# Kernel tuning notes

Measured on AMD Instinct MI355X. Metric: run time of the kernel, lower is better.

## Reference

```python
import jax, jax.numpy as jnp
import numpy as np

B, D_IN, UNITS, D_OUT = 16384, 1024, 512, 512
T_END = 0.1  # ODE integrated over t in (0, 0.1)


def setup_inputs() -> dict:
    key = jax.random.key(0)
    ks = jax.random.split(key, 8)
    return {
        "x": jax.random.normal(ks[0], (B, D_IN), dtype=jnp.float32),
        "w_in": jax.random.normal(ks[1], (UNITS, D_IN), dtype=jnp.float32) * 0.02,
        "b_in": jax.random.normal(ks[2], (UNITS,), dtype=jnp.float32) * 0.02,
        "sensory_w": jax.random.normal(ks[3], (UNITS, UNITS), dtype=jnp.float32) * 0.1,
        "sensory_sigma": jax.random.normal(ks[4], (UNITS,), dtype=jnp.float32) * 0.1,
        # tau = rand(units)*0.5 + 0.5  (in [0.5, 1.0])
        "tau": jax.random.uniform(ks[5], (UNITS,), dtype=jnp.float32) * 0.5 + 0.5,
        "readout_w": jax.random.normal(ks[6], (D_OUT, UNITS), dtype=jnp.float32) * 0.02,
        "readout_b": jax.random.normal(ks[7], (D_OUT,), dtype=jnp.float32) * 0.02,
        # liquid_state buffer starts at zeros, expanded to batch
        "states": jnp.zeros((B, UNITS), dtype=jnp.float32),
    }


def reference(x, w_in, b_in, sensory_w, sensory_sigma, tau, readout_w, readout_b, states):
    # input projection: tanh(Linear(x))
    projected = jnp.tanh(x @ w_in.T + b_in)                       # [B, U]
    # sensory activation A = sigmoid(projected @ sensory_w + sigma)
    A = jax.nn.sigmoid(projected @ sensory_w + sensory_sigma)     # [B, U]
    # ODE dy/dt = (-y + A)/tau has the closed-form solution
    #   y(t) = A + (y0 - A) * exp(-t / tau)
    # which is exactly what solve_ivp(RK45) approximates at t=0.1.
    decay = jnp.exp(-T_END / tau)                                 # [U]
    new_states = A + (states - A) * decay                         # [B, U]
    # readout
    output = new_states @ readout_w.T + readout_b                 # [B, D_OUT]
    return (output, new_states)
```

## Files before the change

### kernel.cpp

```cpp
#include <hip/hip_runtime.h>
#include <stdint.h>
#include <math.h>

typedef __bf16 bf16;
typedef __bf16 bf16x8 __attribute__((ext_vector_type(8)));
typedef __bf16 bf16x4 __attribute__((ext_vector_type(4)));
typedef float f32x4 __attribute__((ext_vector_type(4)));

static constexpr int BATCH = 16384;
static constexpr int D_IN  = 1024;
static constexpr int UNITS = 512;
static constexpr int D_OUT = 512;

__device__ __forceinline__ void gll16(const void* g, void* l) {
    __builtin_amdgcn_global_load_lds(
        (const __attribute__((address_space(1))) void*)g,
        (__attribute__((address_space(3))) void*)l,
        16, 0, 0);
}

__global__ __launch_bounds__(256)
void k_prep(const float* __restrict__ w_in, const float* __restrict__ sens_w,
            const float* __restrict__ ro_w,
            bf16* __restrict__ w_in_bf, bf16* __restrict__ sensT, bf16* __restrict__ ro_bf)
{
    __shared__ float tile[32][33];
    const int b = blockIdx.x;
    const int t = threadIdx.x;
    if (b < 512) {
        int i = b * 256 + t;
        f32x4 v = ((const f32x4*)w_in)[i];
        bf16x4 o = { (bf16)v.x, (bf16)v.y, (bf16)v.z, (bf16)v.w };
        ((bf16x4*)w_in_bf)[i] = o;
    } else if (b < 768) {
        int bb = b - 512;
        int bx = bb & 15, by = bb >> 4;
        int tx = t & 31, ty = t >> 5;
        #pragma unroll
        for (int j = ty; j < 32; j += 8)
            tile[j][tx] = sens_w[(size_t)(by * 32 + j) * UNITS + bx * 32 + tx];
        __syncthreads();
        #pragma unroll
        for (int j = ty; j < 32; j += 8)
            sensT[(size_t)(bx * 32 + j) * UNITS + by * 32 + tx] = (bf16)tile[tx][j];
    } else {
        int i = (b - 768) * 256 + t;
        f32x4 v = ((const f32x4*)ro_w)[i];
        bf16x4 o = { (bf16)v.x, (bf16)v.y, (bf16)v.z, (bf16)v.w };
        ((bf16x4*)ro_bf)[i] = o;
    }
}

template<int K, int EPI, bool AF32>
__global__ __launch_bounds__(512, 4)
void k_gemm(const float* __restrict__ Af, const bf16* __restrict__ Ab,
            const bf16* __restrict__ Bw,
            const float* __restrict__ bias,
            const float* __restrict__ tau,
            const float* __restrict__ states,
            float* __restrict__ outF, bf16* __restrict__ outB,
            int M, int N)
{
    __shared__ bf16 sA[2][128 * 32];
    __shared__ bf16 sB[2][128 * 32];

    const int t = threadIdx.x;
    const int ntiles = N >> 7;
    const int nwg = gridDim.x;
    const int d = blockIdx.x;
    const int bid = (d & 7) * (nwg >> 3) + (d >> 3);
    const int mtile = bid / ntiles;
    const int ntile = bid % ntiles;
    const int m0 = mtile << 7, n0 = ntile << 7;

    const int lane = t & 63;
    const int wave = t >> 6;
    const int wr = (wave >> 1) * 32;
    const int wc = (wave & 1) * 64;
    const int l15 = lane & 15;
    const int lk  = (lane >> 4) * 8;

    f32x4 acc[2][4];
    #pragma unroll
    for (int m = 0; m < 2; ++m)
        #pragma unroll
        for (int n = 0; n < 4; ++n)
            acc[m][n] = (f32x4){0.f, 0.f, 0.f, 0.f};

    const int brow = t >> 2, bk8 = (t & 3) * 8;
    const float* agp = AF32 ? (Af + (size_t)(m0 + brow) * K + bk8) : nullptr;
    const bf16*  abp = AF32 ? nullptr : (Ab + (size_t)(m0 + brow) * K + bk8);
    const bf16*  bbp = Bw + (size_t)(n0 + brow) * K + bk8;

    if constexpr (AF32) {
        f32x4 v0 = ((const f32x4*)agp)[0];
        f32x4 v1 = ((const f32x4*)agp)[1];
        bf16x8 w = { (bf16)v0.x, (bf16)v0.y, (bf16)v0.z, (bf16)v0.w,
                     (bf16)v1.x, (bf16)v1.y, (bf16)v1.z, (bf16)v1.w };
        *(bf16x8*)&sA[0][t * 8] = w;
    } else {
        gll16(abp, &sA[0][t * 8]);
    }
    gll16(bbp, &sB[0][t * 8]);
    __syncthreads();

    int cur = 0;
    for (int kt = 0; kt < K; kt += 32) {
        const int nxt = kt + 32;
        f32x4 v0, v1;
        if (nxt < K) {
            if constexpr (AF32) {
                v0 = ((const f32x4*)(agp + nxt))[0];
                v1 = ((const f32x4*)(agp + nxt))[1];
            } else {
                gll16(abp + nxt, &sA[cur ^ 1][t * 8]);
            }
            gll16(bbp + nxt, &sB[cur ^ 1][t * 8]);
        }
        bf16x8 afr[2], bfr[4];
        #pragma unroll
        for (int m = 0; m < 2; ++m)
            afr[m] = *(const bf16x8*)&sA[cur][(wr + m * 16 + l15) * 32 + lk];
        #pragma unroll
        for (int n = 0; n < 4; ++n)
            bfr[n] = *(const bf16x8*)&sB[cur][(wc + n * 16 + l15) * 32 + lk];
        #pragma unroll
        for (int m = 0; m < 2; ++m)
            #pragma unroll
            for (int n = 0; n < 4; ++n)
                acc[m][n] = __builtin_amdgcn_mfma_f32_16x16x32_bf16(
                                afr[m], bfr[n], acc[m][n], 0, 0, 0);
        if (nxt < K) {
            if constexpr (AF32) {
                bf16x8 w = { (bf16)v0.x, (bf16)v0.y, (bf16)v0.z, (bf16)v0.w,
                             (bf16)v1.x, (bf16)v1.y, (bf16)v1.z, (bf16)v1.w };
                *(bf16x8*)&sA[cur ^ 1][t * 8] = w;
            }
        }
        __syncthreads();
        cur ^= 1;
    }

    const int rbase = m0 + wr + ((lane >> 4) << 2);
    const int cbase = n0 + wc + l15;
    #pragma unroll
    for (int n = 0; n < 4; ++n) {
        const int gc = cbase + n * 16;
        const float bv = bias[gc];
        float dec = 0.f;
        if constexpr (EPI == 2) dec = __expf(-0.1f / tau[gc]);
        #pragma unroll
        for (int m = 0; m < 2; ++m) {
            #pragma unroll
            for (int r = 0; r < 4; ++r) {
                const int gr = rbase + m * 16 + r;
                float v = acc[m][n][r] + bv;
                if constexpr (EPI == 1) {
                    float tv = 1.0f - 2.0f / (1.0f + __expf(2.0f * v));
                    outB[(size_t)gr * N + gc] = (bf16)tv;
                } else if constexpr (EPI == 2) {
                    float a = 1.0f / (1.0f + __expf(-v));
                    float s = states[(size_t)gr * N + gc];
                    outF[(size_t)gr * N + gc] = a + (s - a) * dec;
                } else {
                    outF[(size_t)gr * N + gc] = v;
                }
            }
        }
    }
}

extern "C" void kernel_launch(void* const* d_in, const int* in_sizes, int n_in,
                              void* d_out, int out_size, void* d_ws, size_t ws_size,
                              hipStream_t stream) {
    const float* x        = (const float*)d_in[0];
    const float* w_in     = (const float*)d_in[1];
    const float* b_in     = (const float*)d_in[2];
    const float* sens_w   = (const float*)d_in[3];
    const float* sens_sig = (const float*)d_in[4];
    const float* tau      = (const float*)d_in[5];
    const float* ro_w     = (const float*)d_in[6];
    const float* ro_b     = (const float*)d_in[7];
    const float* states   = (const float*)d_in[8];

    float* out    = (float*)d_out;
    float* new_st = out + (size_t)BATCH * D_OUT;
    bf16*  proj   = (bf16*)d_out;

    bf16* w_in_bf = (bf16*)d_ws;
    bf16* sensT   = w_in_bf + (size_t)UNITS * D_IN;
    bf16* ro_bf   = sensT + (size_t)UNITS * UNITS;

    k_prep<<<1024, 256, 0, stream>>>(w_in, sens_w, ro_w, w_in_bf, sensT, ro_bf);

    k_gemm<1024, 1, true><<<(BATCH / 128) * (UNITS / 128), 512, 0, stream>>>(
        x, nullptr, w_in_bf, b_in, nullptr, nullptr, nullptr, proj, BATCH, UNITS);

    k_gemm<512, 2, false><<<(BATCH / 128) * (UNITS / 128), 512, 0, stream>>>(
        nullptr, proj, sensT, sens_sig, tau, states, new_st, nullptr, BATCH, UNITS);

    k_gemm<512, 3, true><<<(BATCH / 128) * (D_OUT / 128), 512, 0, stream>>>(
        new_st, nullptr, ro_bf, ro_b, nullptr, nullptr, out, nullptr, BATCH, D_OUT);
}
```

Before: 88.59 us.

## Stage fp32 A tiles directly to LDS with swizzle, convert to bf16 at fragment load

For GEMMs whose A operand is fp32, global rows are now copied straight into shared memory with async global-to-LDS loads, using an XOR swizzle on 16-byte chunks. The bf16 conversion moves to the point where fragments are read from shared memory. This removes the register round-trip and the VGPR pressure of holding prefetched fp32 values across the MFMA loop, so loads for the next tile can overlap compute. In exchange it doubles the A-tile shared memory footprint, which may lower occupancy, and repeats the conversion for every wave that reads a row.

```diff
diff --git a/kernel.cpp b/kernel.cpp
--- a/kernel.cpp
+++ b/kernel.cpp
@@ -61,7 +61,8 @@
             float* __restrict__ outF, bf16* __restrict__ outB,
             int M, int N)
 {
-    __shared__ bf16 sA[2][128 * 32];
+    constexpr int ABPB = AF32 ? (128 * 32 * 4) : (128 * 32 * 2);
+    __shared__ __align__(16) char sAraw[2][ABPB];
     __shared__ bf16 sB[2][128 * 32];
 
     const int t = threadIdx.x;
@@ -88,55 +89,58 @@
             acc[m][n] = (f32x4){0.f, 0.f, 0.f, 0.f};
 
     const int brow = t >> 2, bk8 = (t & 3) * 8;
-    const float* agp = AF32 ? (Af + (size_t)(m0 + brow) * K + bk8) : nullptr;
-    const bf16*  abp = AF32 ? nullptr : (Ab + (size_t)(m0 + brow) * K + bk8);
-    const bf16*  bbp = Bw + (size_t)(n0 + brow) * K + bk8;
-
-    if constexpr (AF32) {
-        f32x4 v0 = ((const f32x4*)agp)[0];
-        f32x4 v1 = ((const f32x4*)agp)[1];
-        bf16x8 w = { (bf16)v0.x, (bf16)v0.y, (bf16)v0.z, (bf16)v0.w,
-                     (bf16)v1.x, (bf16)v1.y, (bf16)v1.z, (bf16)v1.w };
-        *(bf16x8*)&sA[0][t * 8] = w;
-    } else {
-        gll16(abp, &sA[0][t * 8]);
-    }
-    gll16(bbp, &sB[0][t * 8]);
+    const bf16* bbp = Bw + (size_t)(n0 + brow) * K + bk8;
+    const int ar  = t >> 3;
+    const int aqs = (((t & 7) ^ (ar & 7)) << 4);
+    const char* ag0 = (const char*)Af + (size_t)(m0 + ar) * K * 4 + aqs;
+    const char* ag1 = (const char*)Af + (size_t)(m0 + 64 + ar) * K * 4 + aqs;
+    const bf16* abp = Ab + (size_t)(m0 + brow) * K + bk8;
+
+    auto STAGE = [&](int buf, int kt) {
+        if constexpr (AF32) {
+            gll16(ag0 + (size_t)kt * 4, &sAraw[buf][t * 16]);
+            gll16(ag1 + (size_t)kt * 4, &sAraw[buf][8192 + t * 16]);
+        } else {
+            gll16(abp + kt, &((bf16*)sAraw[buf])[t * 8]);
+        }
+        gll16(bbp + kt, &sB[buf][t * 8]);
+    };
+
+    STAGE(0, 0);
     __syncthreads();
 
     int cur = 0;
     for (int kt = 0; kt < K; kt += 32) {
-        const int nxt = kt + 32;
-        f32x4 v0, v1;
-        if (nxt < K) {
-            if constexpr (AF32) {
-                v0 = ((const f32x4*)(agp + nxt))[0];
-                v1 = ((const f32x4*)(agp + nxt))[1];
-            } else {
-                gll16(abp + nxt, &sA[cur ^ 1][t * 8]);
+        if (kt + 32 < K) STAGE(cur ^ 1, kt + 32);
+
+        bf16x8 afr[2], bfr[4];
+        if constexpr (AF32) {
+            #pragma unroll
+            for (int m = 0; m < 2; ++m) {
+                const int r = wr + m * 16 + l15;
+                const int s = (r & 7) << 4;
+                const char* rb = &sAraw[cur][r * 128];
+                f32x4 h0 = *(const f32x4*)(rb + ((lk * 4) ^ s));
+                f32x4 h1 = *(const f32x4*)(rb + ((lk * 4 + 16) ^ s));
+                afr[m] = (bf16x8){ (bf16)h0.x, (bf16)h0.y, (bf16)h0.z, (bf16)h0.w,
+                                   (bf16)h1.x, (bf16)h1.y, (bf16)h1.z, (bf16)h1.w };
             }
-            gll16(bbp + nxt, &sB[cur ^ 1][t * 8]);
+        } else {
+            #pragma unroll
+            for (int m = 0; m < 2; ++m)
+                afr[m] = *(const bf16x8*)&((const bf16*)sAraw[cur])[(wr + m * 16 + l15) * 32 + lk];
         }
-        bf16x8 afr[2], bfr[4];
-        #pragma unroll
-        for (int m = 0; m < 2; ++m)
-            afr[m] = *(const bf16x8*)&sA[cur][(wr + m * 16 + l15) * 32 + lk];
         #pragma unroll
         for (int n = 0; n < 4; ++n)
             bfr[n] = *(const bf16x8*)&sB[cur][(wc + n * 16 + l15) * 32 + lk];
+
         #pragma unroll
         for (int m = 0; m < 2; ++m)
             #pragma unroll
             for (int n = 0; n < 4; ++n)
                 acc[m][n] = __builtin_amdgcn_mfma_f32_16x16x32_bf16(
                                 afr[m], bfr[n], acc[m][n], 0, 0, 0);
-        if (nxt < K) {
-            if constexpr (AF32) {
-                bf16x8 w = { (bf16)v0.x, (bf16)v0.y, (bf16)v0.z, (bf16)v0.w,
-                             (bf16)v1.x, (bf16)v1.y, (bf16)v1.z, (bf16)v1.w };
-                *(bf16x8*)&sA[cur ^ 1][t * 8] = w;
-            }
-        }
+
         __syncthreads();
         cur ^= 1;
     }
```

Result: no change. 89.60 us (+1.1%).
